# Kernel optimization log

Hardware: AMD Instinct MI355X
Metric: run time of the kernel (lower is better)

The kernel has to match this reference:

```python
import jax, jax.numpy as jnp
import numpy as np

N = 1_000_000
C = 128
NBINS = 15


def setup_inputs() -> dict:
    key = jax.random.key(0)
    k1, k2 = jax.random.split(key)
    logits = jax.random.normal(k1, (N, C), dtype=jnp.float32)
    labels = jax.random.randint(k2, (N,), 0, C, dtype=jnp.int64)
    return {"logits": logits, "labels": labels}


def reference(logits, labels):
    n = logits.shape[0]
    probs = jax.nn.softmax(logits, axis=1)
    confidences = jnp.max(probs, axis=1)                      # [N]
    predictions = jnp.argmax(probs, axis=1)                   # [N]
    accuracies = (predictions == labels).astype(jnp.float32)  # [N]

    # Equal-count (adaptive) bin edges: interp(linspace(0,N,nbins+1), arange(N), sort(conf))
    sorted_conf = jnp.sort(confidences)
    q = jnp.linspace(0.0, float(n), NBINS + 1)
    edges = jnp.interp(q, jnp.arange(n, dtype=jnp.float32), sorted_conf)  # [NBINS+1]

    # Bin i covers (edges[i], edges[i+1]] to match conf.gt(lower) & conf.le(upper).
    idx = jnp.searchsorted(edges[1:-1], confidences, side="left")  # [N] in [0, NBINS-1]
    valid = (confidences > edges[0]) & (confidences <= edges[-1])
    idx = jnp.where(valid, idx, NBINS)  # dump out-of-range into extra segment

    cnt = jax.ops.segment_sum(jnp.ones_like(confidences), idx, num_segments=NBINS + 1)[:NBINS]
    csum = jax.ops.segment_sum(confidences, idx, num_segments=NBINS + 1)[:NBINS]
    asum = jax.ops.segment_sum(accuracies, idx, num_segments=NBINS + 1)[:NBINS]

    prop = cnt / jnp.float32(n)
    safe = jnp.maximum(cnt, 1.0)
    gap = jnp.abs(csum / safe - asum / safe)
    ece = jnp.sum(jnp.where(cnt > 0, gap * prop, 0.0))
    return ece.reshape(1)
```

## Files before the change

kernel.cpp:

```cpp
#include <hip/hip_runtime.h>
#include <hip/hip_bf16.h>
#include <cstdint>

#define NROWS 1000000
#define NCLS  128
#define NBINS 15

#define FBASE 0x3B000000u
#define NB    73728
#define SCAN_T 1024
#define PER   (NB / SCAN_T)

#define OFF_CONF   0u
#define OFF_ACC    4000000u
#define OFF_HIST   5000000u
#define OFF_SUB    5294912u
#define OFF_PART   5417792u
#define OFF_TGTB   5614400u
#define OFF_TGTL   5614520u
#define OFF_EDGES  5614640u
#define ZERO_BYTES (OFF_PART - OFF_HIST)

#define DPP_FMAX(v, CTRL) { int _t = __builtin_amdgcn_update_dpp(                 \
        __float_as_int(v), __float_as_int(v), CTRL, 0xF, 0xF, false);             \
        (v) = fmaxf((v), __int_as_float(_t)); }
#define DPP_FADD(v, CTRL) { int _t = __builtin_amdgcn_update_dpp(                 \
        0, __float_as_int(v), CTRL, 0xF, 0xF, true);                              \
        (v) = (v) + __int_as_float(_t); }
#define CTRL_SHR1 0x111
#define CTRL_SHR2 0x112
#define CTRL_SHR4 0x114
#define CTRL_SHR8 0x118

__global__ __launch_bounds__(256) void k_row(const float* __restrict__ logits,
                                             const int* __restrict__ labels,
                                             float* __restrict__ conf,
                                             unsigned char* __restrict__ acc,
                                             unsigned int* __restrict__ histT)
{
    const int lane = threadIdx.x & 63;
    const int wv   = threadIdx.x >> 6;
    const int g    = lane >> 4;
    const int l16  = lane & 15;
    const int wbase = blockIdx.x * 32 + wv * 8;
    const float4* lg4 = reinterpret_cast<const float4*>(logits);

#pragma unroll
    for (int half = 0; half < 2; half++) {
        const int row = wbase + half * 4 + g;
        const float4 v0 = lg4[row * 32 + l16];
        const float4 v1 = lg4[row * 32 + 16 + l16];
        const int lab = labels[row];

        float m = fmaxf(fmaxf(fmaxf(v0.x, v0.y), fmaxf(v0.z, v0.w)),
                        fmaxf(fmaxf(v1.x, v1.y), fmaxf(v1.z, v1.w)));
        DPP_FMAX(m, CTRL_SHR1); DPP_FMAX(m, CTRL_SHR2);
        DPP_FMAX(m, CTRL_SHR4); DPP_FMAX(m, CTRL_SHR8);

        float s = __expf(v0.x) + __expf(v0.y) + __expf(v0.z) + __expf(v0.w)
                + __expf(v1.x) + __expf(v1.y) + __expf(v1.z) + __expf(v1.w);
        DPP_FADD(s, CTRL_SHR1); DPP_FADD(s, CTRL_SHR2);
        DPP_FADD(s, CTRL_SHR4); DPP_FADD(s, CTRL_SHR8);

        const bool hiHalf = (lab & 64) != 0;
        const float cx = hiHalf ? v1.x : v0.x;
        const float cy = hiHalf ? v1.y : v0.y;
        const float cz = hiHalf ? v1.z : v0.z;
        const float cw = hiHalf ? v1.w : v0.w;
        const int e = lab & 3;
        const float cand = (e == 0) ? cx : (e == 1) ? cy : (e == 2) ? cz : cw;
        float lv = (((lab >> 2) & 15) == l16) ? cand : __int_as_float(0xFF800000);
        DPP_FMAX(lv, CTRL_SHR1); DPP_FMAX(lv, CTRL_SHR2);
        DPP_FMAX(lv, CTRL_SHR4); DPP_FMAX(lv, CTRL_SHR8);

        if (l16 == 15) {
            const float c = __expf(m) / s;
            conf[row] = c;
            acc[row]  = (lv == m) ? 1u : 0u;
            int ub = (int)(__float_as_uint(c) - FBASE);
            int b  = ub >> 10;
            b = b < 0 ? 0 : (b >= NB ? NB - 1 : b);
            atomicAdd(&histT[(b % PER) * 1024 + b / PER], 1u);
        }
    }
}

__device__ __forceinline__ unsigned int rank_of(int s)
{
    if (s == 0)  return 0u;
    if (s == 29) return (unsigned int)(NROWS - 1);
    int i = (s + 1) >> 1;
    unsigned int k = (unsigned int)((long long)i * NROWS / 15);
    return k + ((s & 1) ? 0u : 1u);
}

__global__ __launch_bounds__(SCAN_T) void k_scan(const unsigned int* __restrict__ histT,
                                                 int* __restrict__ tgtb,
                                                 int* __restrict__ tgtl)
{
    __shared__ unsigned int v[SCAN_T];
    const int t = threadIdx.x;
    unsigned int s = 0;
    for (int j = 0; j < PER; j++) s += histT[j * 1024 + t];
    v[t] = s;
    __syncthreads();
    for (int off = 1; off < SCAN_T; off <<= 1) {
        unsigned int x = (t >= off) ? v[t - off] : 0u;
        __syncthreads();
        v[t] += x;
        __syncthreads();
    }
    const unsigned int run0 = v[t] - s;
    for (int s2 = 0; s2 < 30; s2++) {
        unsigned int r = rank_of(s2);
        if (r >= run0 && r < run0 + s) {
            unsigned int run = run0;
            for (int j = 0; j < PER; j++) {
                unsigned int c = histT[j * 1024 + t];
                if (r < run + c) { tgtb[s2] = t * PER + j; tgtl[s2] = (int)(r - run); break; }
                run += c;
            }
        }
    }
}

__global__ __launch_bounds__(256) void k_subhist(const float* __restrict__ conf,
                                                 const int* __restrict__ tgtb,
                                                 unsigned int* __restrict__ sub)
{
    __shared__ int tb[32];
    if (threadIdx.x < 32) tb[threadIdx.x] = (threadIdx.x < 30) ? tgtb[threadIdx.x] : 0x7FFFFFFF;
    __syncthreads();
    const int stride = gridDim.x * blockDim.x;
    for (int i = blockIdx.x * blockDim.x + threadIdx.x; i < NROWS / 4; i += stride) {
        float4 c4 = reinterpret_cast<const float4*>(conf)[i];
        float cv[4] = {c4.x, c4.y, c4.z, c4.w};
#pragma unroll
        for (int e = 0; e < 4; e++) {
            int ub = (int)(__float_as_uint(cv[e]) - FBASE);
            int b  = ub >> 10;
            b = b < 0 ? 0 : (b >= NB ? NB - 1 : b);
            int lo10 = ub & 1023;
            int lo = (tb[15] < b) ? 16 : 0;
            lo += (tb[lo + 7] < b) ? 8 : 0;
            lo += (tb[lo + 3] < b) ? 4 : 0;
            lo += (tb[lo + 1] < b) ? 2 : 0;
            lo += (tb[lo]     < b) ? 1 : 0;
            if (tb[lo] == b) atomicAdd(&sub[lo * 1024 + lo10], 1u);
        }
    }
}

__global__ __launch_bounds__(1024) void k_edges(const unsigned int* __restrict__ sub,
                        const int* __restrict__ tgtb,
                        const int* __restrict__ tgtl,
                        float* __restrict__ edges)
{
    __shared__ float val[32];
    __shared__ int tb[30], rep[30];
    if (threadIdx.x < 30) tb[threadIdx.x] = tgtb[threadIdx.x];
    __syncthreads();
    if (threadIdx.x < 30) {
        int r = 0;
        while (tb[r] != tb[threadIdx.x]) r++;
        rep[threadIdx.x] = r;
    }
    __syncthreads();
    const int g = threadIdx.x >> 5;
    const int k = threadIdx.x & 31;
    if (g < 30) {
        const unsigned int local = (unsigned int)tgtl[g];
        unsigned int cs[32];
        unsigned int csum = 0;
        const unsigned int* p = sub + rep[g] * 1024 + k * 32;
#pragma unroll
        for (int j = 0; j < 32; j++) { cs[j] = p[j]; csum += cs[j]; }
        unsigned int incl = csum;
#pragma unroll
        for (int off = 1; off < 32; off <<= 1) {
            unsigned int x = __shfl_up(incl, off);
            if (k >= off) incl += x;
        }
        const unsigned int excl = incl - csum;
        if (local >= excl && local < excl + csum) {
            unsigned int run = excl;
            int subidx = 0;
#pragma unroll
            for (int j = 0; j < 32; j++) {
                if (local >= run && local < run + cs[j]) subidx = k * 32 + j;
                run += cs[j];
            }
            unsigned int bits = FBASE + ((unsigned int)tb[g] << 10) + (unsigned int)subidx;
            val[g] = __uint_as_float(bits);
        }
    }
    __syncthreads();
    if (threadIdx.x == 0) {
        edges[0]  = val[0];
        edges[15] = val[29];
        for (int i = 1; i <= 14; i++) {
            double q = (double)i * (double)NROWS / 15.0;
            long long kk = (long long)i * NROWS / 15;
            double f = q - (double)kk;
            edges[i] = (float)((1.0 - f) * (double)val[2 * i - 1] + f * (double)val[2 * i]);
        }
    }
}

__global__ __launch_bounds__(256) void k_bin(const float* __restrict__ conf,
                                             const unsigned char* __restrict__ acc,
                                             const float* __restrict__ edges,
                                             float* __restrict__ partial)
{
    __shared__ float se[16];
    __shared__ float sl[3][64 * 17];
    if (threadIdx.x < 16) se[threadIdx.x] = edges[threadIdx.x];
    for (int i = threadIdx.x; i < 3 * 64 * 17; i += 256) (&sl[0][0])[i] = 0.f;
    __syncthreads();

    const int slice = threadIdx.x & 63;
    const int stride = gridDim.x * blockDim.x;
    for (int i = blockIdx.x * blockDim.x + threadIdx.x; i < NROWS / 4; i += stride) {
        float4 c4 = reinterpret_cast<const float4*>(conf)[i];
        uchar4 a4 = reinterpret_cast<const uchar4*>(acc)[i];
        float cv[4] = {c4.x, c4.y, c4.z, c4.w};
        unsigned char av[4] = {a4.x, a4.y, a4.z, a4.w};
#pragma unroll
        for (int e = 0; e < 4; e++) {
            float v = cv[e];
            if (v > se[0] && v <= se[15]) {
                int idx = 0;
#pragma unroll
                for (int j = 1; j <= 14; j++) idx += (se[j] < v) ? 1 : 0;
                atomicAdd(&sl[0][slice * 17 + idx], 1.0f);
                atomicAdd(&sl[1][slice * 17 + idx], v);
                atomicAdd(&sl[2][slice * 17 + idx], (float)av[e]);
            }
        }
    }
    __syncthreads();
    if (threadIdx.x < 48) {
        const int a = threadIdx.x >> 4, b = threadIdx.x & 15;
        float sum = 0.f;
        for (int s = 0; s < 64; s++) sum += sl[a][s * 17 + b];
        partial[(a * 16 + b) * 1024 + blockIdx.x] = sum;
    }
}

__global__ __launch_bounds__(1024) void k_final(const float* __restrict__ partial,
                                                float* __restrict__ out)
{
    __shared__ double tot[48];
    const int w    = threadIdx.x >> 6;
    const int lane = threadIdx.x & 63;
#pragma unroll
    for (int c = 0; c < 3; c++) {
        const int j = w * 3 + c;
        double s = 0.0;
#pragma unroll
        for (int i = 0; i < 16; i++) s += (double)partial[j * 1024 + i * 64 + lane];
#pragma unroll
        for (int d = 1; d < 64; d <<= 1) s += __shfl_xor(s, d);
        if (lane == 0) tot[j] = s;
    }
    __syncthreads();
    if (threadIdx.x == 0) {
        double ece = 0.0;
        for (int b = 0; b < NBINS; b++) {
            double cnt = tot[b];
            if (cnt > 0.0) {
                double safe = cnt < 1.0 ? 1.0 : cnt;
                double gap  = fabs(tot[16 + b] / safe - tot[32 + b] / safe);
                ece += gap * (cnt / (double)NROWS);
            }
        }
        out[0] = (float)ece;
    }
}

extern "C" void kernel_launch(void* const* d_in, const int* in_sizes, int n_in,
                              void* d_out, int out_size, void* d_ws, size_t ws_size,
                              hipStream_t stream)
{
    const float* logits = (const float*)d_in[0];
    const int*   labels = (const int*)d_in[1];
    char* ws = (char*)d_ws;

    float*         conf  = (float*)(ws + OFF_CONF);
    unsigned char* acc   = (unsigned char*)(ws + OFF_ACC);
    unsigned int*  histT = (unsigned int*)(ws + OFF_HIST);
    unsigned int*  sub   = (unsigned int*)(ws + OFF_SUB);
    float*         part  = (float*)(ws + OFF_PART);
    int*           tgtb  = (int*)(ws + OFF_TGTB);
    int*           tgtl  = (int*)(ws + OFF_TGTL);
    float*         edges = (float*)(ws + OFF_EDGES);

    hipMemsetAsync(ws + OFF_HIST, 0, ZERO_BYTES, stream);

    k_row<<<NROWS / 32, 256, 0, stream>>>(logits, labels, conf, acc, histT);
    k_scan<<<1, SCAN_T, 0, stream>>>(histT, tgtb, tgtl);
    k_subhist<<<1024, 256, 0, stream>>>(conf, tgtb, sub);
    k_edges<<<1, 1024, 0, stream>>>(sub, tgtb, tgtl, edges);
    k_bin<<<1024, 256, 0, stream>>>(conf, acc, edges, part);
    k_final<<<1, 1024, 0, stream>>>(part, (float*)d_out);
}
```

Measured before the change: 215.0 us.

## Use contiguous histogram layout, wave-shuffle scan, and fewer binning blocks

New measurement: 210.0 us. -2.3%, faster.

```diff
diff --git a/kernel.cpp b/kernel.cpp
--- a/kernel.cpp
+++ b/kernel.cpp
@@ -16,9 +16,9 @@
 #define OFF_HIST   5000000u
 #define OFF_SUB    5294912u
 #define OFF_PART   5417792u
-#define OFF_TGTB   5614400u
-#define OFF_TGTL   5614520u
-#define OFF_EDGES  5614640u
+#define OFF_TGTB   5466944u
+#define OFF_TGTL   5467064u
+#define OFF_EDGES  5467184u
 #define ZERO_BYTES (OFF_PART - OFF_HIST)
 
 #define DPP_FMAX(v, CTRL) { int _t = __builtin_amdgcn_update_dpp(                 \
@@ -36,7 +36,7 @@
                                              const int* __restrict__ labels,
                                              float* __restrict__ conf,
                                              unsigned char* __restrict__ acc,
-                                             unsigned int* __restrict__ histT)
+                                             unsigned int* __restrict__ hist)
 {
     const int lane = threadIdx.x & 63;
     const int wv   = threadIdx.x >> 6;
@@ -80,7 +80,7 @@
             int ub = (int)(__float_as_uint(c) - FBASE);
             int b  = ub >> 10;
             b = b < 0 ? 0 : (b >= NB ? NB - 1 : b);
-            atomicAdd(&histT[(b % PER) * 1024 + b / PER], 1u);
+            atomicAdd(&hist[b], 1u);
         }
     }
 }
@@ -94,29 +94,40 @@
     return k + ((s & 1) ? 0u : 1u);
 }
 
-__global__ __launch_bounds__(SCAN_T) void k_scan(const unsigned int* __restrict__ histT,
+__global__ __launch_bounds__(SCAN_T) void k_scan(const unsigned int* __restrict__ hist,
                                                  int* __restrict__ tgtb,
                                                  int* __restrict__ tgtl)
 {
-    __shared__ unsigned int v[SCAN_T];
+    __shared__ unsigned int wtot[16], wpre[16];
     const int t = threadIdx.x;
+    const int w = t >> 6, lane = t & 63;
+
+    const uint4* h4 = reinterpret_cast<const uint4*>(hist + t * PER);
     unsigned int s = 0;
-    for (int j = 0; j < PER; j++) s += histT[j * 1024 + t];
-    v[t] = s;
-    __syncthreads();
-    for (int off = 1; off < SCAN_T; off <<= 1) {
-        unsigned int x = (t >= off) ? v[t - off] : 0u;
-        __syncthreads();
-        v[t] += x;
-        __syncthreads();
-    }
-    const unsigned int run0 = v[t] - s;
+#pragma unroll
+    for (int j = 0; j < PER / 4; j++) { uint4 u = h4[j]; s += u.x + u.y + u.z + u.w; }
+
+    unsigned int incl = s;
+#pragma unroll
+    for (int off = 1; off < 64; off <<= 1) {
+        unsigned int x = __shfl_up(incl, off);
+        if (lane >= off) incl += x;
+    }
+    if (lane == 63) wtot[w] = incl;
+    __syncthreads();
+    if (t == 0) {
+        unsigned int run = 0;
+        for (int i = 0; i < 16; i++) { wpre[i] = run; run += wtot[i]; }
+    }
+    __syncthreads();
+    const unsigned int run0 = wpre[w] + incl - s;
+
     for (int s2 = 0; s2 < 30; s2++) {
         unsigned int r = rank_of(s2);
         if (r >= run0 && r < run0 + s) {
             unsigned int run = run0;
             for (int j = 0; j < PER; j++) {
-                unsigned int c = histT[j * 1024 + t];
+                unsigned int c = hist[t * PER + j];
                 if (r < run + c) { tgtb[s2] = t * PER + j; tgtl[s2] = (int)(r - run); break; }
                 run += c;
             }
@@ -243,7 +254,7 @@
         const int a = threadIdx.x >> 4, b = threadIdx.x & 15;
         float sum = 0.f;
         for (int s = 0; s < 64; s++) sum += sl[a][s * 17 + b];
-        partial[(a * 16 + b) * 1024 + blockIdx.x] = sum;
+        partial[(a * 16 + b) * 256 + blockIdx.x] = sum;
     }
 }
 
@@ -253,12 +264,10 @@
     __shared__ double tot[48];
     const int w    = threadIdx.x >> 6;
     const int lane = threadIdx.x & 63;
-#pragma unroll
-    for (int c = 0; c < 3; c++) {
-        const int j = w * 3 + c;
+    for (int j = w; j < 48; j += 16) {
         double s = 0.0;
 #pragma unroll
-        for (int i = 0; i < 16; i++) s += (double)partial[j * 1024 + i * 64 + lane];
+        for (int i = 0; i < 4; i++) s += (double)partial[j * 256 + i * 64 + lane];
 #pragma unroll
         for (int d = 1; d < 64; d <<= 1) s += __shfl_xor(s, d);
         if (lane == 0) tot[j] = s;
@@ -288,7 +297,7 @@
 
     float*         conf  = (float*)(ws + OFF_CONF);
     unsigned char* acc   = (unsigned char*)(ws + OFF_ACC);
-    unsigned int*  histT = (unsigned int*)(ws + OFF_HIST);
+    unsigned int*  hist  = (unsigned int*)(ws + OFF_HIST);
     unsigned int*  sub   = (unsigned int*)(ws + OFF_SUB);
     float*         part  = (float*)(ws + OFF_PART);
     int*           tgtb  = (int*)(ws + OFF_TGTB);
@@ -297,10 +306,10 @@
 
     hipMemsetAsync(ws + OFF_HIST, 0, ZERO_BYTES, stream);
 
-    k_row<<<NROWS / 32, 256, 0, stream>>>(logits, labels, conf, acc, histT);
-    k_scan<<<1, SCAN_T, 0, stream>>>(histT, tgtb, tgtl);
+    k_row<<<NROWS / 32, 256, 0, stream>>>(logits, labels, conf, acc, hist);
+    k_scan<<<1, SCAN_T, 0, stream>>>(hist, tgtb, tgtl);
     k_subhist<<<1024, 256, 0, stream>>>(conf, tgtb, sub);
     k_edges<<<1, 1024, 0, stream>>>(sub, tgtb, tgtl, edges);
-    k_bin<<<1024, 256, 0, stream>>>(conf, acc, edges, part);
+    k_bin<<<256, 256, 0, stream>>>(conf, acc, edges, part);
     k_final<<<1, 1024, 0, stream>>>(part, (float*)d_out);
 }
```
